# Kernel tuning notes

Hardware: AMD Instinct MI355X
Metric: run time of the kernel (lower is better)

The kernel has to match this reference:

```python
import jax, jax.numpy as jnp
import numpy as np
import jax.scipy.linalg as jsl

K = 4           # num_hops + 1
N = 4096        # nodes
D = 256         # in_dim == out_dim
S = 32          # subspace_dim
ETA = 0.5
EPS = 0.5


def setup_inputs() -> dict:
    key = jax.random.key(0)
    k1, k2, k3 = jax.random.split(key, 3)
    hops = jax.random.normal(k1, (K, N, D), dtype=jnp.float32)
    A = (jax.random.uniform(k2, (N, N)) < 0.01).astype(jnp.float32)
    A = jnp.maximum(A, A.T)
    A = jnp.fill_diagonal(A, 1.0, inplace=False)
    deg = A.sum(axis=1)
    L = jnp.diag(deg) - A  # graph Laplacian
    # orthonormal subspace bases via QR, as in __init__
    raw = jax.random.normal(k3, (K, D, S), dtype=jnp.float32)
    q, _ = jnp.linalg.qr(raw)
    U = q[:, :, :S]
    hop_weights = jnp.ones((K,), dtype=jnp.float32) / K
    threshold = jnp.full((D,), 0.05, dtype=jnp.float32)
    lambda_lap = jnp.asarray(0.1, dtype=jnp.float32)
    return {"hops": hops, "adj_mask": A, "L": L, "U": U,
            "hop_weights": hop_weights, "threshold": threshold,
            "lambda_lap": lambda_lap}


def reference(hops, adj_mask, L, U, hop_weights, threshold, lambda_lap):
    n = hops.shape[1]
    s = U.shape[-1]
    w = jax.nn.softmax(hop_weights, axis=0)
    mask_add = (1.0 - adj_mask) * -1e9  # [n, n]
    I_s = jnp.eye(s, dtype=hops.dtype)
    agg_total = jnp.zeros((hops.shape[2], n), dtype=hops.dtype)  # [d, n]
    coeff = s / (n * EPS ** 2)
    for k in range(K):  # small fixed hop count
        Uk = U[k]                      # [d, s]
        Zk = Uk.T @ hops[k].T          # [s, n]
        M_k = I_s + coeff * (Zk @ Zk.T)  # [s, s]
        cf = jsl.cho_factor(M_k)
        M_inv = jsl.cho_solve(cf, I_s)   # Cholesky inverse
        MZ = M_inv @ Zk                  # [s, n]
        scores = Zk.T @ MZ + mask_add    # [n, n] Mahalanobis-style attention
        alpha = jax.nn.softmax(scores, axis=1)
        grad_k = Uk @ (MZ @ alpha.T)     # [d, n]
        agg_total = agg_total + w[k] * grad_k
    H_agg = agg_total.T                  # [n, d]
    lap_grad = lambda_lap * (L @ H_agg)
    H_half = hops[0] + ETA * H_agg - ETA * lap_grad
    # soft-threshold (proximal step); in_dim == out_dim so no proj
    H_out = jnp.sign(H_half) * jax.nn.relu(jnp.abs(H_half) - threshold[None, :])
    # orthogonality regularizer over subspace bases
    orth_loss = jnp.asarray(0.0, dtype=hops.dtype)
    for k in range(K):
        UkTUk = U[k].T @ U[k]
        orth_loss = orth_loss + ((UkTUk - I_s) ** 2).sum()
        for l in range(k + 1, K):
            orth_loss = orth_loss + ((U[k].T @ U[l]) ** 2).sum()
    lap_smooth = jnp.sum(H_out * (L @ H_out))  # trace(H^T L H)
    return (H_out, orth_loss, lap_smooth, jax.lax.stop_gradient(w))
```

## Files before the change

### kernel.cpp

```cpp
#include <hip/hip_runtime.h>
#include <cstddef>

typedef unsigned short ushortt;
typedef unsigned int uintt;

static constexpr int Nn = 4096;
static constexpr int Dd = 256;
static constexpr int Ss = 32;
static constexpr int Kk = 4;
static constexpr int CAP = 160;
static constexpr float kEta   = 0.5f;
static constexpr float kCoeff = 0.03125f;

__device__ __forceinline__ float waveReduceSum(float v){
  #pragma unroll
  for (int off = 32; off > 0; off >>= 1) v += __shfl_down(v, off, 64);
  return v;
}
__device__ __forceinline__ float blo(uintt u){ return __uint_as_float(u << 16); }
__device__ __forceinline__ float bhi(uintt u){ return __uint_as_float(u & 0xffff0000u); }
__device__ __forceinline__ ushortt f2b(float x){
  uintt u = __float_as_uint(x);
  uintt r = (u + 0x7fffu + ((u >> 16) & 1u)) >> 16;
  return (ushortt)r;
}
__device__ __forceinline__ float b2f(ushortt u){ return __uint_as_float(((uintt)u) << 16); }

__global__ __launch_bounds__(256) void build_kernel(const float* __restrict__ A,
                                                    const float* __restrict__ hw,
                                                    int* __restrict__ deg,
                                                    int* __restrict__ colx,
                                                    float* __restrict__ out){
  int i = blockIdx.x, tid = threadIdx.x;
  if (i == 0 && tid == 0){
    out[1048576] = 0.f;
    out[1048577] = 0.f;
    float a0=hw[0], a1=hw[1], a2=hw[2], a3=hw[3];
    float mx = fmaxf(fmaxf(a0,a1), fmaxf(a2,a3));
    float e0=expf(a0-mx), e1=expf(a1-mx), e2=expf(a2-mx), e3=expf(a3-mx);
    float s = e0+e1+e2+e3;
    out[1048578]=e0/s; out[1048579]=e1/s; out[1048580]=e2/s; out[1048581]=e3/s;
  }
  int lane = tid & 63, w = tid >> 6;
  __shared__ int wbuf[4][96];
  __shared__ int wcnt[4];
  const float4* row4 = (const float4*)(A + (size_t)i * Nn);
  int cnt = 0;
  int base = w * 256;
  #pragma unroll
  for (int it = 0; it < 4; it++){
    int c4 = base + it * 64 + lane;
    float4 v = row4[c4];
    int f0 = (v.x != 0.f), f1 = (v.y != 0.f), f2 = (v.z != 0.f), f3 = (v.w != 0.f);
    int nf = f0 + f1 + f2 + f3;
    int pre = nf;
    #pragma unroll
    for (int off = 1; off < 64; off <<= 1){
      int o = __shfl_up(pre, off, 64);
      if (lane >= off) pre += o;
    }
    int tot = __shfl(pre, 63, 64);
    int pos = cnt + pre - nf;
    int j0 = c4 * 4;
    if (f0){ if (pos < 96) wbuf[w][pos] = j0;     pos++; }
    if (f1){ if (pos < 96) wbuf[w][pos] = j0 + 1; pos++; }
    if (f2){ if (pos < 96) wbuf[w][pos] = j0 + 2; pos++; }
    if (f3){ if (pos < 96) wbuf[w][pos] = j0 + 3; pos++; }
    cnt += tot;
  }
  if (cnt > 96) cnt = 96;
  if (lane == 0) wcnt[w] = cnt;
  __syncthreads();
  int off = 0;
  for (int ww = 0; ww < w; ww++) off += wcnt[ww];
  int total = wcnt[0] + wcnt[1] + wcnt[2] + wcnt[3];
  for (int idx = lane; idx < cnt; idx += 64){
    int p = off + idx;
    if (p < CAP) colx[(size_t)i * CAP + p] = wbuf[w][idx];
  }
  if (tid == 0) deg[i] = (total < CAP) ? total : CAP;
}

__global__ __launch_bounds__(256) void z_kernel(const float* __restrict__ hops,
                                                const float* __restrict__ U,
                                                float* __restrict__ Zt4,
                                                float* __restrict__ Ubt){
  int b = blockIdx.x;
  int k = b >> 9;
  int i0 = (b & 511) * 8;
  __shared__ float Us[Ss][260];
  for (int t = threadIdx.x; t < Dd * Ss; t += 256){
    int s = t & 31, d = t >> 5;
    Us[s][d] = U[(size_t)k * Dd * Ss + t];
  }
  __syncthreads();
  int s = threadIdx.x & 31, ii = threadIdx.x >> 5;
  int i = i0 + ii;
  const float4* h4 = (const float4*)(hops + ((size_t)k * Nn + i) * Dd);
  const float4* u4 = (const float4*)(&Us[s][0]);
  float acc = 0.f;
  #pragma unroll 8
  for (int dq = 0; dq < 64; dq++){
    float4 h = h4[dq];
    float4 u = u4[dq];
    acc += h.x*u.x + h.y*u.y + h.z*u.z + h.w*u.w;
  }
  Zt4[(size_t)i * 128 + k * 32 + s] = acc;
  if (b < 128){
    int idx = b * 256 + threadIdx.x;
    int c = idx >> 8, d = idx & 255;
    int kk = c >> 5, s2 = c & 31;
    Ubt[idx] = U[(size_t)kk * Dd * Ss + (size_t)d * Ss + s2];
  }
}

__global__ __launch_bounds__(256) void mpart_kernel(const float* __restrict__ Zt4,
                                                    float* __restrict__ Mpart){
  int b = blockIdx.x;
  int k = b >> 4, ch = b & 15;
  int i0 = ch * 256;
  __shared__ float zs[256][33];
  for (int t = threadIdx.x; t < 256 * 32; t += 256){
    int ii = t >> 5, s = t & 31;
    zs[ii][s] = Zt4[(size_t)(i0 + ii) * 128 + k * 32 + s];
  }
  __syncthreads();
  int tid = threadIdx.x;
  int s2 = tid & 31, s1b = tid >> 5;
  float a0=0.f, a1=0.f, a2=0.f, a3=0.f;
  for (int ii = 0; ii < 256; ii++){
    float zc = zs[ii][s2];
    a0 = fmaf(zs[ii][s1b],      zc, a0);
    a1 = fmaf(zs[ii][8 + s1b],  zc, a1);
    a2 = fmaf(zs[ii][16 + s1b], zc, a2);
    a3 = fmaf(zs[ii][24 + s1b], zc, a3);
  }
  float* outp = Mpart + (size_t)b * 1024;
  outp[0 * 256 + tid] = a0;
  outp[1 * 256 + tid] = a1;
  outp[2 * 256 + tid] = a2;
  outp[3 * 256 + tid] = a3;
}

__global__ __launch_bounds__(256) void inv_kernel(const float* __restrict__ Mpart,
                                                  float* __restrict__ Minv){
  __shared__ float Msh[4][32][33];
  int tid = threadIdx.x;
  for (int e = tid; e < 4096; e += 256){
    int k = e >> 10, rc = e & 1023;
    float s = 0.f;
    for (int ch = 0; ch < 16; ch++) s += Mpart[(size_t)(k * 16 + ch) * 1024 + rc];
    int r = rc >> 5, c = rc & 31;
    Msh[k][r][c] = kCoeff * s + ((r == c) ? 1.f : 0.f);
  }
  __syncthreads();
  int k = tid >> 6, lane = tid & 63, r = lane & 31, half = lane >> 5;
  float a[32];
  #pragma unroll
  for (int j = 0; j < 32; j++) a[j] = half ? ((r == j) ? 1.f : 0.f) : Msh[k][r][j];
  #pragma unroll
  for (int p = 0; p < 32; p++){
    float app = __shfl(a[p], p, 64);
    float pinv = 1.f / app;
    float f = __shfl(a[p], r, 64);
    #pragma unroll
    for (int j = 0; j < 32; j++){
      float pr = __shfl(a[j], p + (half << 5), 64) * pinv;
      a[j] = (r == p) ? pr : fmaf(-f, pr, a[j]);
    }
  }
  if (half){
    #pragma unroll
    for (int j = 0; j < 32; j++) Minv[(size_t)k * 1024 + r * 32 + j] = a[j];
  }
}

__global__ __launch_bounds__(256) void mz_kernel(const float* __restrict__ Zt4,
                                                 const float* __restrict__ Minv,
                                                 ushortt* __restrict__ MZb){
  int b = blockIdx.x;
  int k = b >> 7;
  int i0 = (b & 127) * 32;
  __shared__ float mi[32][33];
  __shared__ float zs[32][33];
  for (int t = threadIdx.x; t < 1024; t += 256){
    int ii = t >> 5, s2 = t & 31;
    mi[ii][s2] = Minv[(size_t)k * 1024 + t];
    zs[ii][s2] = Zt4[(size_t)(i0 + ii) * 128 + k * 32 + s2];
  }
  __syncthreads();
  int s = threadIdx.x & 31;
  for (int rr = 0; rr < 4; rr++){
    int ii = rr * 8 + (threadIdx.x >> 5);
    float acc = 0.f;
    #pragma unroll
    for (int s2 = 0; s2 < 32; s2++) acc = fmaf(mi[s][s2], zs[ii][s2], acc);
    MZb[(size_t)(i0 + ii) * 128 + k * 32 + s] = f2b(acc);
  }
}

__global__ __launch_bounds__(256) void agg_kernel(const float* __restrict__ Zt4,
                                                  const ushortt* __restrict__ MZb,
                                                  const float* __restrict__ wvec,
                                                  const int* __restrict__ deg,
                                                  const int* __restrict__ colx,
                                                  float* __restrict__ Vw){
  int i = blockIdx.x, tid = threadIdx.x;
  int lane = tid & 63, k = tid >> 6;
  __shared__ int cols[CAP];
  __shared__ __align__(16) float zi[128];
  __shared__ float sc[4][CAP + 8];
  int m = deg[i];
  if (tid < 128) zi[tid] = Zt4[(size_t)i * 128 + tid];
  for (int t = tid; t < m; t += 256) cols[t] = colx[(size_t)i * CAP + t];
  __syncthreads();

  float zr[32];
  {
    const float4* z4 = (const float4*)(&zi[k * 32]);
    #pragma unroll
    for (int q = 0; q < 8; q++){
      float4 z = z4[q];
      zr[q*4+0]=z.x; zr[q*4+1]=z.y; zr[q*4+2]=z.z; zr[q*4+3]=z.w;
    }
  }
  float lmax = -3.0e38f;
  for (int t = lane; t < m; t += 64){
    int j = cols[t];
    const uint4* rp = (const uint4*)(MZb + ((size_t)j * 128 + k * 32));
    uint4 q0 = rp[0], q1 = rp[1], q2 = rp[2], q3 = rp[3];
    float acc = 0.f;
    acc += blo(q0.x)*zr[0] + bhi(q0.x)*zr[1] + blo(q0.y)*zr[2] + bhi(q0.y)*zr[3];
    acc += blo(q0.z)*zr[4] + bhi(q0.z)*zr[5] + blo(q0.w)*zr[6] + bhi(q0.w)*zr[7];
    acc += blo(q1.x)*zr[8] + bhi(q1.x)*zr[9] + blo(q1.y)*zr[10]+ bhi(q1.y)*zr[11];
    acc += blo(q1.z)*zr[12]+ bhi(q1.z)*zr[13]+ blo(q1.w)*zr[14]+ bhi(q1.w)*zr[15];
    acc += blo(q2.x)*zr[16]+ bhi(q2.x)*zr[17]+ blo(q2.y)*zr[18]+ bhi(q2.y)*zr[19];
    acc += blo(q2.z)*zr[20]+ bhi(q2.z)*zr[21]+ blo(q2.w)*zr[22]+ bhi(q2.w)*zr[23];
    acc += blo(q3.x)*zr[24]+ bhi(q3.x)*zr[25]+ blo(q3.y)*zr[26]+ bhi(q3.y)*zr[27];
    acc += blo(q3.z)*zr[28]+ bhi(q3.z)*zr[29]+ blo(q3.w)*zr[30]+ bhi(q3.w)*zr[31];
    sc[k][t] = acc;
    lmax = fmaxf(lmax, acc);
  }
  #pragma unroll
  for (int off = 32; off > 0; off >>= 1) lmax = fmaxf(lmax, __shfl_xor(lmax, off, 64));
  float lsum = 0.f;
  for (int t = lane; t < m; t += 64){
    float e = __expf(sc[k][t] - lmax);
    sc[k][t] = e;
    lsum += e;
  }
  #pragma unroll
  for (int off = 32; off > 0; off >>= 1) lsum += __shfl_xor(lsum, off, 64);
  float scale = wvec[k] / lsum;

  int c8 = lane & 7, h = lane >> 3;
  float a0 = 0.f, a1 = 0.f, a2 = 0.f, a3 = 0.f;
  #pragma unroll 2
  for (int t = h; t < m; t += 8){
    int j = cols[t];
    uint2 u = *(const uint2*)(MZb + ((size_t)j * 128 + k * 32 + c8 * 4));
    float e = sc[k][t];
    a0 = fmaf(blo(u.x), e, a0);
    a1 = fmaf(bhi(u.x), e, a1);
    a2 = fmaf(blo(u.y), e, a2);
    a3 = fmaf(bhi(u.y), e, a3);
  }
  #pragma unroll
  for (int off = 8; off < 64; off <<= 1){
    a0 += __shfl_xor(a0, off, 64);
    a1 += __shfl_xor(a1, off, 64);
    a2 += __shfl_xor(a2, off, 64);
    a3 += __shfl_xor(a3, off, 64);
  }
  if (h == 0){
    float4 v4 = make_float4(a0 * scale, a1 * scale, a2 * scale, a3 * scale);
    *(float4*)(Vw + (size_t)i * 128 + k * 32 + c8 * 4) = v4;
  }
}

__global__ __launch_bounds__(256) void houtfused_kernel(const float* __restrict__ Vw,
                                                        const float* __restrict__ Ubt,
                                                        const float* __restrict__ hops0,
                                                        const float* __restrict__ thr,
                                                        const float* __restrict__ lam_ptr,
                                                        const int* __restrict__ deg,
                                                        const int* __restrict__ colx,
                                                        float* __restrict__ out,
                                                        ushortt* __restrict__ Hb){
  int i0 = blockIdx.x * 16;
  int tid = threadIdx.x;
  int lane = tid & 63, w = tid >> 6;
  __shared__ float Cs[16][132];
  __shared__ int cols_s[16][CAP];
  __shared__ int deg_s[16];
  for (int rr = w; rr < 16; rr += 4){
    int i = i0 + rr;
    int m = deg[i];
    if (lane == 0) deg_s[rr] = m;
    for (int t = lane; t < m; t += 64) cols_s[rr][t] = colx[(size_t)i * CAP + t];
  }
  __syncthreads();
  float lam = lam_ptr[0];
  int nb2 = lane >> 5;
  int c32 = lane & 31;
  for (int rr = w; rr < 16; rr += 4){
    int i = i0 + rr;
    int m = deg_s[rr];
    float4 acc = make_float4(0.f, 0.f, 0.f, 0.f);
    for (int t = nb2; t < m; t += 2){
      int j = cols_s[rr][t];
      float4 v = ((const float4*)(Vw + (size_t)j * 128))[c32];
      acc.x += v.x; acc.y += v.y; acc.z += v.z; acc.w += v.w;
    }
    acc.x += __shfl_xor(acc.x, 32, 64);
    acc.y += __shfl_xor(acc.y, 32, 64);
    acc.z += __shfl_xor(acc.z, 32, 64);
    acc.w += __shfl_xor(acc.w, 32, 64);
    if (nb2 == 0){
      float4 self = ((const float4*)(Vw + (size_t)i * 128))[c32];
      float ca = kEta * (1.f - lam * (float)m);
      float cb = kEta * lam;
      float4 o;
      o.x = fmaf(ca, self.x, cb * acc.x);
      o.y = fmaf(ca, self.y, cb * acc.y);
      o.z = fmaf(ca, self.z, cb * acc.z);
      o.w = fmaf(ca, self.w, cb * acc.w);
      *(float4*)(&Cs[rr][c32 * 4]) = o;
    }
  }
  __syncthreads();
  int d4 = tid & 63, g = tid >> 6;
  float4 acc[4];
  #pragma unroll
  for (int r = 0; r < 4; r++) acc[r] = make_float4(0.f, 0.f, 0.f, 0.f);
  #pragma unroll 2
  for (int c = 0; c < 128; c++){
    float4 ub = ((const float4*)(Ubt + (size_t)c * 256))[d4];
    #pragma unroll
    for (int r = 0; r < 4; r++){
      float cs = Cs[g * 4 + r][c];
      acc[r].x = fmaf(cs, ub.x, acc[r].x);
      acc[r].y = fmaf(cs, ub.y, acc[r].y);
      acc[r].z = fmaf(cs, ub.z, acc[r].z);
      acc[r].w = fmaf(cs, ub.w, acc[r].w);
    }
  }
  float4 th = ((const float4*)thr)[d4];
  #pragma unroll
  for (int r = 0; r < 4; r++){
    int i = i0 + g * 4 + r;
    float4 hp = ((const float4*)(hops0 + (size_t)i * 256))[d4];
    float hx = hp.x + acc[r].x, hy = hp.y + acc[r].y;
    float hz = hp.z + acc[r].z, hw = hp.w + acc[r].w;
    float4 o;
    o.x = copysignf(fmaxf(fabsf(hx) - th.x, 0.f), hx);
    o.y = copysignf(fmaxf(fabsf(hy) - th.y, 0.f), hy);
    o.z = copysignf(fmaxf(fabsf(hz) - th.z, 0.f), hz);
    o.w = copysignf(fmaxf(fabsf(hw) - th.w, 0.f), hw);
    ((float4*)(out + (size_t)i * 256))[d4] = o;
    ushort4 hb;
    hb.x = f2b(o.x); hb.y = f2b(o.y); hb.z = f2b(o.z); hb.w = f2b(o.w);
    *((ushort4*)(Hb + (size_t)i * 256 + d4 * 4)) = hb;
  }
}

__global__ __launch_bounds__(256) void lap_kernel(const float* __restrict__ Hout,
                                                  const ushortt* __restrict__ Hb,
                                                  const int* __restrict__ deg,
                                                  const int* __restrict__ colx,
                                                  float* __restrict__ lap_part){
  int b = blockIdx.x;
  int i = b >> 1, half = b & 1;
  int tid = threadIdx.x;
  int dl = tid & 127, g = tid >> 7;
  int d = half * 128 + dl;
  __shared__ int cols[CAP];
  int m = deg[i];
  for (int t = tid; t < m; t += 256) cols[t] = colx[(size_t)i * CAP + t];
  __syncthreads();
  float nb = 0.f;
  #pragma unroll 8
  for (int t = g; t < m; t += 2)
    nb += b2f(Hb[(size_t)cols[t] * 256 + d]);
  float hi = Hout[(size_t)i * 256 + d];
  float part = -hi * nb;
  if (g == 0) part = fmaf((float)m * hi, hi, part);
  part = waveReduceSum(part);
  __shared__ float red[4];
  if ((tid & 63) == 0) red[tid >> 6] = part;
  __syncthreads();
  if (tid == 0) lap_part[b] = red[0] + red[1] + red[2] + red[3];
}

__global__ __launch_bounds__(256) void orth_kernel(const float* __restrict__ U,
                                                   const float* __restrict__ lap_part,
                                                   float* __restrict__ out){
  int tid = threadIdx.x;
  if (blockIdx.x == 40){
    float s = 0.f;
    const float4* p4 = (const float4*)lap_part;
    #pragma unroll
    for (int q = 0; q < 8; q++){
      float4 v = p4[q * 256 + tid];
      s += v.x + v.y + v.z + v.w;
    }
    s = waveReduceSum(s);
    __shared__ float redl[4];
    if ((tid & 63) == 0) redl[tid >> 6] = s;
    __syncthreads();
    if (tid == 0) out[1048577] = redl[0] + redl[1] + redl[2] + redl[3];
    return;
  }
  int g = blockIdx.x * 256 + tid;
  int pair = g >> 10;
  int idx = g & 1023;
  int s1 = idx >> 5, s2 = idx & 31;
  const int pk_[10] = {0,0,0,0,1,1,1,2,2,3};
  const int pl_[10] = {0,1,2,3,1,2,3,2,3,3};
  int pk = pk_[pair], pl = pl_[pair];
  const float* Uk = U + (size_t)pk * Dd * Ss;
  const float* Ul = U + (size_t)pl * Dd * Ss;
  float dot = 0.f;
  for (int d = 0; d < Dd; d++) dot += Uk[d * Ss + s1] * Ul[d * Ss + s2];
  float val = dot - ((pk == pl && s1 == s2) ? 1.f : 0.f);
  val *= val;
  val = waveReduceSum(val);
  __shared__ float red[4];
  if ((tid & 63) == 0) red[tid >> 6] = val;
  __syncthreads();
  if (tid == 0) atomicAdd(out + 1048576, red[0] + red[1] + red[2] + red[3]);
}

extern "C" void kernel_launch(void* const* d_in, const int* in_sizes, int n_in,
                              void* d_out, int out_size, void* d_ws, size_t ws_size,
                              hipStream_t stream)
{
  const float* hops = (const float*)d_in[0];
  const float* A    = (const float*)d_in[1];
  const float* L    = (const float*)d_in[2];
  const float* U    = (const float*)d_in[3];
  const float* hw   = (const float*)d_in[4];
  const float* thr  = (const float*)d_in[5];
  const float* lam  = (const float*)d_in[6];
  (void)L; (void)in_sizes; (void)n_in; (void)out_size; (void)ws_size;

  float* out = (float*)d_out;
  float* ws  = (float*)d_ws;

  float*   Zt4   = ws;
  float*   Vw    = ws + 524288;
  ushortt* MZb   = (ushortt*)(ws + 1572864);
  ushortt* Hb    = (ushortt*)(ws + 1835008);
  float*   Ubt   = ws + 2359296;
  float*   Mpart = ws + 2392064;
  float*   Minv  = ws + 2457600;
  int*     deg   = (int*)(ws + 2461696);
  int*     colx  = (int*)(ws + 2465792);
  float*   lapp  = ws + 3121152;

  float* w_out = out + 1048578;

  build_kernel    <<<Nn, 256, 0, stream>>>(A, hw, deg, colx, out);
  z_kernel        <<<Kk*512, 256, 0, stream>>>(hops, U, Zt4, Ubt);
  mpart_kernel    <<<Kk*16, 256, 0, stream>>>(Zt4, Mpart);
  inv_kernel      <<<1, 256, 0, stream>>>(Mpart, Minv);
  mz_kernel       <<<Kk*128, 256, 0, stream>>>(Zt4, Minv, MZb);
  agg_kernel      <<<Nn, 256, 0, stream>>>(Zt4, MZb, w_out, deg, colx, Vw);
  houtfused_kernel<<<256, 256, 0, stream>>>(Vw, Ubt, hops, thr, lam, deg, colx, out, Hb);
  lap_kernel      <<<2*Nn, 256, 0, stream>>>(out, Hb, deg, colx, lapp);
  orth_kernel     <<<41, 256, 0, stream>>>(U, lapp, out);
}
```

Baseline: 329.6 us.

## Split Laplacian neighbor gather out of fused hout kernel into per-node kernel

The sparse neighbor gather of Vw rows, previously done inside the 256-block hout kernel, moves to a new 4096-block kernel that writes the blended coefficients to a workspace buffer. The hout kernel then only loads those coefficients and runs the dense projection. The aim is more parallelism for the latency-bound gather. The cost is an extra launch plus a 2 MB intermediate write and read.

```diff
diff --git a/kernel.cpp b/kernel.cpp
--- a/kernel.cpp
+++ b/kernel.cpp
@@ -278,55 +278,44 @@
   }
 }
 
-__global__ __launch_bounds__(256) void houtfused_kernel(const float* __restrict__ Vw,
+__global__ __launch_bounds__(256) void gatherv_kernel(const float* __restrict__ Vw,
+                                                      const float* __restrict__ lam_ptr,
+                                                      const int* __restrict__ deg,
+                                                      const int* __restrict__ colx,
+                                                      float* __restrict__ cVc){
+  int i = blockIdx.x, tid = threadIdx.x;
+  int c = tid & 127, g = tid >> 7;
+  __shared__ int cols[CAP];
+  __shared__ float vred[2][128];
+  int m = deg[i];
+  for (int t = tid; t < m; t += 256) cols[t] = colx[(size_t)i * CAP + t];
+  __syncthreads();
+  float acc = 0.f;
+  #pragma unroll 8
+  for (int t = g; t < m; t += 2)
+    acc += Vw[(size_t)cols[t] * 128 + c];
+  vred[g][c] = acc;
+  __syncthreads();
+  if (tid < 128){
+    float nb = vred[0][tid] + vred[1][tid];
+    float lam = lam_ptr[0];
+    float self = Vw[(size_t)i * 128 + tid];
+    cVc[(size_t)i * 128 + tid] = kEta * (1.f - lam * (float)m) * self + kEta * lam * nb;
+  }
+}
+
+__global__ __launch_bounds__(256) void houtblend_kernel(const float* __restrict__ cVc,
                                                         const float* __restrict__ Ubt,
                                                         const float* __restrict__ hops0,
                                                         const float* __restrict__ thr,
-                                                        const float* __restrict__ lam_ptr,
-                                                        const int* __restrict__ deg,
-                                                        const int* __restrict__ colx,
                                                         float* __restrict__ out,
                                                         ushortt* __restrict__ Hb){
   int i0 = blockIdx.x * 16;
   int tid = threadIdx.x;
-  int lane = tid & 63, w = tid >> 6;
   __shared__ float Cs[16][132];
-  __shared__ int cols_s[16][CAP];
-  __shared__ int deg_s[16];
-  for (int rr = w; rr < 16; rr += 4){
-    int i = i0 + rr;
-    int m = deg[i];
-    if (lane == 0) deg_s[rr] = m;
-    for (int t = lane; t < m; t += 64) cols_s[rr][t] = colx[(size_t)i * CAP + t];
-  }
-  __syncthreads();
-  float lam = lam_ptr[0];
-  int nb2 = lane >> 5;
-  int c32 = lane & 31;
-  for (int rr = w; rr < 16; rr += 4){
-    int i = i0 + rr;
-    int m = deg_s[rr];
-    float4 acc = make_float4(0.f, 0.f, 0.f, 0.f);
-    for (int t = nb2; t < m; t += 2){
-      int j = cols_s[rr][t];
-      float4 v = ((const float4*)(Vw + (size_t)j * 128))[c32];
-      acc.x += v.x; acc.y += v.y; acc.z += v.z; acc.w += v.w;
-    }
-    acc.x += __shfl_xor(acc.x, 32, 64);
-    acc.y += __shfl_xor(acc.y, 32, 64);
-    acc.z += __shfl_xor(acc.z, 32, 64);
-    acc.w += __shfl_xor(acc.w, 32, 64);
-    if (nb2 == 0){
-      float4 self = ((const float4*)(Vw + (size_t)i * 128))[c32];
-      float ca = kEta * (1.f - lam * (float)m);
-      float cb = kEta * lam;
-      float4 o;
-      o.x = fmaf(ca, self.x, cb * acc.x);
-      o.y = fmaf(ca, self.y, cb * acc.y);
-      o.z = fmaf(ca, self.z, cb * acc.z);
-      o.w = fmaf(ca, self.w, cb * acc.w);
-      *(float4*)(&Cs[rr][c32 * 4]) = o;
-    }
+  for (int t = tid; t < 16 * 128; t += 256){
+    int ii = t >> 7, c = t & 127;
+    Cs[ii][c] = cVc[(size_t)(i0 + ii) * 128 + c];
   }
   __syncthreads();
   int d4 = tid & 63, g = tid >> 6;
@@ -449,6 +438,7 @@
 
   float*   Zt4   = ws;
   float*   Vw    = ws + 524288;
+  float*   cVc   = ws + 1048576;
   ushortt* MZb   = (ushortt*)(ws + 1572864);
   ushortt* Hb    = (ushortt*)(ws + 1835008);
   float*   Ubt   = ws + 2359296;
@@ -466,7 +456,8 @@
   inv_kernel      <<<1, 256, 0, stream>>>(Mpart, Minv);
   mz_kernel       <<<Kk*128, 256, 0, stream>>>(Zt4, Minv, MZb);
   agg_kernel      <<<Nn, 256, 0, stream>>>(Zt4, MZb, w_out, deg, colx, Vw);
-  houtfused_kernel<<<256, 256, 0, stream>>>(Vw, Ubt, hops, thr, lam, deg, colx, out, Hb);
+  gatherv_kernel  <<<Nn, 256, 0, stream>>>(Vw, lam, deg, colx, cVc);
+  houtblend_kernel<<<256, 256, 0, stream>>>(cVc, Ubt, hops, thr, out, Hb);
   lap_kernel      <<<2*Nn, 256, 0, stream>>>(out, Hb, deg, colx, lapp);
   orth_kernel     <<<41, 256, 0, stream>>>(U, lapp, out);
 }
```

Result: faster. 311.7 us (-5.4%).
